# Performance work log

Hardware: AMD Instinct MI355X
Metric: run time of the kernel (lower is better)

The kernel has to match this reference:

```python
import jax, jax.numpy as jnp
import numpy as np


def setup_inputs() -> dict:
    key = jax.random.key(0)
    k1, k2, *kw = jax.random.split(key, 12)
    N, E = 10000, 320000
    D_IN, D_HID, D_EMB, D_PRED = 2, 128, 256, 128

    def lin(k, fan_in, fan_out):
        bound = 1.0 / np.sqrt(fan_in)
        kw_, kb_ = jax.random.split(k)
        W = jax.random.uniform(kw_, (fan_in, fan_out), jnp.float32, -bound, bound)
        b = jax.random.uniform(kb_, (fan_out,), jnp.float32, -bound, bound)
        return W, b

    W1, b1 = lin(kw[0], D_IN, D_HID)
    W2, b2 = lin(kw[1], D_HID, D_EMB)
    Wp1, bp1 = lin(kw[2], D_EMB, D_PRED)
    Wp2, bp2 = lin(kw[3], D_PRED, 1)

    src = jax.random.randint(k1, (E,), 0, N, dtype=jnp.int32)
    dst = jax.random.randint(k2, (E,), 0, N, dtype=jnp.int32)
    return {
        "W1": W1, "b1": b1, "W2": W2, "b2": b2,
        "Wp1": Wp1, "bp1": bp1, "Wp2": Wp2, "bp2": bp2,
        "src": src, "dst": dst, "num_nodes": N,
    }


def reference(W1, b1, W2, b2, Wp1, bp1, Wp2, bp2, src, dst, num_nodes):
    N = num_nodes
    E = src.shape[0]
    ones = jnp.ones((E,), jnp.float32)
    # node features = [in_degree, out_degree]  -> [N, 2]
    in_deg = jax.ops.segment_sum(ones, dst, num_segments=N)
    out_deg = jax.ops.segment_sum(ones, src, num_segments=N)
    x = jnp.stack([in_deg, out_deg], axis=1)

    def gcn_agg(h):
        # sum of messages from source nodes into destination nodes (SpMM-like)
        return jax.ops.segment_sum(h[src], dst, num_segments=N)

    h = jax.nn.relu(gcn_agg(x) @ W1 + b1)        # [N, 128]
    h = gcn_agg(h) @ W2 + b2                     # [N, 256]
    h = jax.nn.relu(h)
    graph_embedding = jnp.sum(h, axis=0)         # [256] (dgl.sum_nodes, single graph)
    m = jax.nn.relu(graph_embedding @ Wp1 + bp1)
    metric = m @ Wp2 + bp2                       # [1]
    return (graph_embedding, metric)
```

## Files before the change

### kernel.cpp

```cpp
#include <hip/hip_runtime.h>

#define N_NODES 10000
#define CAPLOG 7
#define CAP 128
#define NPART 16
#define NBH 128
#define TBH 512
#define TSTRIDE 132
#define HB 128

__global__ __launch_bounds__(TBH) void hist_kernel(const int* __restrict__ src,
                                                   const int* __restrict__ dst,
                                                   uchar2* __restrict__ cnt,
                                                   float* __restrict__ ge_p,
                                                   float* __restrict__ m,
                                                   unsigned int* __restrict__ done,
                                                   int E) {
  __shared__ unsigned int hist[N_NODES];
  const int tid = threadIdx.x, bid = blockIdx.x;
  for (int i = tid; i < N_NODES; i += TBH) hist[i] = 0;
  if (bid < NPART && tid < 256) ge_p[(bid << 8) + tid] = 0.f;
  if (bid == NPART && tid < HB) m[tid] = 0.f;
  if (bid == NPART && tid == HB) *done = 0u;
  __syncthreads();
  const int chunk = (E + NBH - 1) / NBH;
  const int e0 = bid * chunk, e1 = min(E, e0 + chunk);
  for (int e = e0 + tid; e < e1; e += TBH) {
    atomicAdd(&hist[dst[e]], 1u);
    atomicAdd(&hist[src[e]], 0x10000u);
  }
  __syncthreads();
  uchar2* outb = cnt + (size_t)bid * N_NODES;
  for (int i = tid; i < N_NODES; i += TBH) {
    const unsigned v = hist[i];
    outb[i] = make_uchar2((unsigned char)(v & 0xFFFFu), (unsigned char)(v >> 16));
  }
}

__global__ __launch_bounds__(256) void scan_kernel(const uchar2* __restrict__ cnt,
                                                   unsigned char* __restrict__ off,
                                                   unsigned int* __restrict__ pack) {
  const int n = blockIdx.x * 256 + threadIdx.x;
  if (n >= N_NODES) return;
  unsigned run_in = 0, run_out = 0;
#pragma unroll 16
  for (int b = 0; b < NBH; ++b) {
    const uchar2 c = cnt[(size_t)b * N_NODES + n];
    off[(size_t)b * N_NODES + n] = (unsigned char)run_in;
    run_in += c.x;
    run_out += c.y;
  }
  pack[n] = run_in | (run_out << 16);
}

__global__ __launch_bounds__(TBH) void scatter_kernel(const int* __restrict__ src,
                                                      const int* __restrict__ dst,
                                                      const unsigned char* __restrict__ off,
                                                      unsigned short* __restrict__ slots,
                                                      int E) {
  __shared__ unsigned int cur[N_NODES];
  const int tid = threadIdx.x, bid = blockIdx.x;
  const unsigned char* ob = off + (size_t)bid * N_NODES;
  for (int i = tid; i < N_NODES; i += TBH) cur[i] = ob[i];
  __syncthreads();
  const int chunk = (E + NBH - 1) / NBH;
  const int e0 = bid * chunk, e1 = min(E, e0 + chunk);
  for (int e = e0 + tid; e < e1; e += TBH) {
    int d = dst[e];
    unsigned idx = atomicAdd(&cur[d], 1u);
    if (idx < CAP) slots[(d << CAPLOG) + idx] = (unsigned short)src[e];
  }
}

__global__ __launch_bounds__(256) void agg1_kernel(const unsigned int* __restrict__ pack,
                                                   const unsigned short* __restrict__ slots,
                                                   unsigned int* __restrict__ a) {
  const int tid = threadIdx.x;
  const int hw = tid >> 5, hl = tid & 31;
  const int node = blockIdx.x * 8 + hw;
  const int deg = min((int)(pack[node] & 0xFFFFu), CAP);
  const int base = node << CAPLOG;
  unsigned acc = 0u;
  for (int e = hl; e < deg; e += 32) acc += pack[slots[base + e]];
#pragma unroll
  for (int off = 16; off > 0; off >>= 1) acc += (unsigned)__shfl_xor((int)acc, off, 32);
  if (hl == 0) a[node] = acc;
}

#define FMA_ROW(aR0, aR1, aR2, aR3, t)                                       \
  aR0 = fmaf(t.x, w0.x, aR0); aR0 = fmaf(t.y, w1.x, aR0);                    \
  aR0 = fmaf(t.z, w2v.x, aR0); aR0 = fmaf(t.w, w3.x, aR0);                   \
  aR1 = fmaf(t.x, w0.y, aR1); aR1 = fmaf(t.y, w1.y, aR1);                    \
  aR1 = fmaf(t.z, w2v.y, aR1); aR1 = fmaf(t.w, w3.y, aR1);                   \
  aR2 = fmaf(t.x, w0.z, aR2); aR2 = fmaf(t.y, w1.z, aR2);                    \
  aR2 = fmaf(t.z, w2v.z, aR2); aR2 = fmaf(t.w, w3.z, aR2);                   \
  aR3 = fmaf(t.x, w0.w, aR3); aR3 = fmaf(t.y, w1.w, aR3);                    \
  aR3 = fmaf(t.z, w2v.w, aR3); aR3 = fmaf(t.w, w3.w, aR3);

__global__ __launch_bounds__(256, 4) void agg2gemm2_kernel(const unsigned int* __restrict__ pack,
                                                           const unsigned short* __restrict__ slots,
                                                           const unsigned int* __restrict__ a,
                                                           const float* __restrict__ W1,
                                                           const float* __restrict__ b1,
                                                           const float* __restrict__ W2,
                                                           const float* __restrict__ b2,
                                                           float* __restrict__ ge_p) {
  __shared__ float2 s_a[16][CAP + 1];
  __shared__ float s_t[16 * TSTRIDE];
  __shared__ float s_red[4][256];
  const int tid = threadIdx.x, bid = blockIdx.x;
  const int hw = tid >> 5, hl = tid & 31;

#pragma unroll
  for (int nn = 0; nn < 2; ++nn) {
    const int row = hw * 2 + nn;
    const int node = bid * 16 + row;
    const int deg = min((int)(pack[node] & 0xFFFFu), CAP);
    const int base = node << CAPLOG;
    for (int e = hl; e < deg; e += 32) {
      const unsigned v = a[slots[base + e]];
      s_a[row][e] = make_float2((float)(v & 0xFFFFu), (float)(v >> 16));
    }
  }

  float w10[4], w11[4], bb[4];
#pragma unroll
  for (int c = 0; c < 4; ++c) {
    w10[c] = W1[4 * hl + c];
    w11[c] = W1[128 + 4 * hl + c];
    bb[c] = b1[4 * hl + c];
  }
  __syncthreads();

#pragma unroll
  for (int nn = 0; nn < 2; ++nn) {
    const int row = hw * 2 + nn;
    const int node = bid * 16 + row;
    const int deg = min((int)(pack[node] & 0xFFFFu), CAP);
    float acc0 = 0.f, acc1 = 0.f, acc2 = 0.f, acc3 = 0.f;
#pragma unroll 4
    for (int j = 0; j < deg; ++j) {
      const float2 av = s_a[row][j];
      acc0 += fmaxf(fmaf(av.x, w10[0], fmaf(av.y, w11[0], bb[0])), 0.f);
      acc1 += fmaxf(fmaf(av.x, w10[1], fmaf(av.y, w11[1], bb[1])), 0.f);
      acc2 += fmaxf(fmaf(av.x, w10[2], fmaf(av.y, w11[2], bb[2])), 0.f);
      acc3 += fmaxf(fmaf(av.x, w10[3], fmaf(av.y, w11[3], bb[3])), 0.f);
    }
    float* tr = s_t + row * TSTRIDE + 4 * hl;
    tr[0] = acc0; tr[1] = acc1; tr[2] = acc2; tr[3] = acc3;
  }
  __syncthreads();

  const int jq = tid & 63, ng = tid >> 6;
  const int j = jq << 2;
  const float* tb = s_t + (ng << 2) * TSTRIDE;
  float4 wc0 = *(const float4*)(W2 + 0 * 256 + j);
  float4 wc1 = *(const float4*)(W2 + 1 * 256 + j);
  float4 wc2 = *(const float4*)(W2 + 2 * 256 + j);
  float4 wc3 = *(const float4*)(W2 + 3 * 256 + j);
  float a00 = 0.f, a01 = 0.f, a02 = 0.f, a03 = 0.f;
  float a10 = 0.f, a11 = 0.f, a12 = 0.f, a13 = 0.f;
  float a20 = 0.f, a21 = 0.f, a22 = 0.f, a23 = 0.f;
  float a30 = 0.f, a31 = 0.f, a32 = 0.f, a33 = 0.f;
#pragma unroll 4
  for (int k = 0; k < 124; k += 4) {
    const float4 wn0 = *(const float4*)(W2 + (k + 4) * 256 + j);
    const float4 wn1 = *(const float4*)(W2 + (k + 5) * 256 + j);
    const float4 wn2 = *(const float4*)(W2 + (k + 6) * 256 + j);
    const float4 wn3 = *(const float4*)(W2 + (k + 7) * 256 + j);
    const float4 t0 = *(const float4*)(tb + 0 * TSTRIDE + k);
    const float4 t1 = *(const float4*)(tb + 1 * TSTRIDE + k);
    const float4 t2 = *(const float4*)(tb + 2 * TSTRIDE + k);
    const float4 t3 = *(const float4*)(tb + 3 * TSTRIDE + k);
    {
      const float4 w0 = wc0, w1 = wc1, w2v = wc2, w3 = wc3;
      FMA_ROW(a00, a01, a02, a03, t0)
      FMA_ROW(a10, a11, a12, a13, t1)
      FMA_ROW(a20, a21, a22, a23, t2)
      FMA_ROW(a30, a31, a32, a33, t3)
    }
    wc0 = wn0; wc1 = wn1; wc2 = wn2; wc3 = wn3;
  }
  {
    const float4 t0 = *(const float4*)(tb + 0 * TSTRIDE + 124);
    const float4 t1 = *(const float4*)(tb + 1 * TSTRIDE + 124);
    const float4 t2 = *(const float4*)(tb + 2 * TSTRIDE + 124);
    const float4 t3 = *(const float4*)(tb + 3 * TSTRIDE + 124);
    const float4 w0 = wc0, w1 = wc1, w2v = wc2, w3 = wc3;
    FMA_ROW(a00, a01, a02, a03, t0)
    FMA_ROW(a10, a11, a12, a13, t1)
    FMA_ROW(a20, a21, a22, a23, t2)
    FMA_ROW(a30, a31, a32, a33, t3)
  }

  const float4 bj = *(const float4*)(b2 + j);
  float4 part;
  part.x = fmaxf(a00 + bj.x, 0.f) + fmaxf(a10 + bj.x, 0.f) +
           fmaxf(a20 + bj.x, 0.f) + fmaxf(a30 + bj.x, 0.f);
  part.y = fmaxf(a01 + bj.y, 0.f) + fmaxf(a11 + bj.y, 0.f) +
           fmaxf(a21 + bj.y, 0.f) + fmaxf(a31 + bj.y, 0.f);
  part.z = fmaxf(a02 + bj.z, 0.f) + fmaxf(a12 + bj.z, 0.f) +
           fmaxf(a22 + bj.z, 0.f) + fmaxf(a32 + bj.z, 0.f);
  part.w = fmaxf(a03 + bj.w, 0.f) + fmaxf(a13 + bj.w, 0.f) +
           fmaxf(a23 + bj.w, 0.f) + fmaxf(a33 + bj.w, 0.f);
  *(float4*)(&s_red[ng][j]) = part;
  __syncthreads();
  const float g = (s_red[0][tid] + s_red[1][tid]) + (s_red[2][tid] + s_red[3][tid]);
  atomicAdd(&ge_p[((bid & (NPART - 1)) << 8) + tid], g);
}

__global__ __launch_bounds__(256) void head_kernel(const float* __restrict__ ge_p,
                                                   const float* __restrict__ Wp1,
                                                   const float* __restrict__ bp1,
                                                   const float* __restrict__ Wp2,
                                                   const float* __restrict__ bp2,
                                                   float* __restrict__ m,
                                                   unsigned int* __restrict__ done,
                                                   float* __restrict__ out) {
  __shared__ float s_r[4];
  __shared__ int s_last;
  const int tid = threadIdx.x, j = blockIdx.x;
  float g = 0.f;
#pragma unroll
  for (int p = 0; p < NPART; ++p) g += ge_p[p * 256 + tid];
  if (j == 0) out[tid] = g;
  float part = g * Wp1[tid * 128 + j];
#pragma unroll
  for (int o = 32; o > 0; o >>= 1) part += __shfl_xor(part, o);
  if ((tid & 63) == 0) s_r[tid >> 6] = part;
  __syncthreads();
  if (tid == 0) {
    const float mj = bp1[j] + (s_r[0] + s_r[1]) + (s_r[2] + s_r[3]);
    atomicAdd(&m[j], mj);
    __threadfence();
    s_last = (atomicAdd(done, 1u) == HB - 1) ? 1 : 0;
  }
  __syncthreads();
  if (!s_last) return;
  float v = 0.f;
  if (tid < 128)
    v = fmaxf(__hip_atomic_load(&m[tid], __ATOMIC_RELAXED, __HIP_MEMORY_SCOPE_AGENT), 0.f) *
        Wp2[tid];
#pragma unroll
  for (int o = 32; o > 0; o >>= 1) v += __shfl_xor(v, o);
  if ((tid & 63) == 0) s_r[tid >> 6] = v;
  __syncthreads();
  if (tid == 0) out[256] = s_r[0] + s_r[1] + bp2[0];
}

extern "C" void kernel_launch(void* const* d_in, const int* in_sizes, int n_in,
                              void* d_out, int out_size, void* d_ws, size_t ws_size,
                              hipStream_t stream) {
  const float* W1 = (const float*)d_in[0];
  const float* b1 = (const float*)d_in[1];
  const float* W2 = (const float*)d_in[2];
  const float* b2 = (const float*)d_in[3];
  const float* Wp1 = (const float*)d_in[4];
  const float* bp1 = (const float*)d_in[5];
  const float* Wp2 = (const float*)d_in[6];
  const float* bp2 = (const float*)d_in[7];
  const int* src = (const int*)d_in[8];
  const int* dst = (const int*)d_in[9];
  const int E = in_sizes[8];
  const int N = N_NODES;

  char* p = (char*)d_ws;
  float* ge_p = (float*)p;               p += (size_t)NPART * 256 * 4;
  float* m = (float*)p;                  p += HB * 4;
  unsigned int* done = (unsigned int*)p; p += 16;
  unsigned int* pack = (unsigned int*)p; p += (size_t)N * 4;
  unsigned int* a = (unsigned int*)p;    p += (size_t)N * 4;
  unsigned short* slots = (unsigned short*)p; p += (size_t)N * CAP * 2;
  uchar2* cnt = (uchar2*)p;              p += (size_t)NBH * N * 2;
  unsigned char* off = (unsigned char*)p;
  float* out = (float*)d_out;

  hist_kernel<<<NBH, TBH, 0, stream>>>(src, dst, cnt, ge_p, m, done, E);
  scan_kernel<<<(N + 255) / 256, 256, 0, stream>>>(cnt, off, pack);
  scatter_kernel<<<NBH, TBH, 0, stream>>>(src, dst, off, slots, E);
  agg1_kernel<<<N / 8, 256, 0, stream>>>(pack, slots, a);
  agg2gemm2_kernel<<<N / 16, 256, 0, stream>>>(pack, slots, a, W1, b1, W2, b2, ge_p);
  head_kernel<<<HB, 256, 0, stream>>>(ge_p, Wp1, bp1, Wp2, bp2, m, done, out);
}
```

Before: 125.4 us.

## Fuse hist, scan, scatter and agg1 into one persistent kernel with grid barriers

After: 159.1 us. 1.27x slower.

```diff
diff --git a/kernel.cpp b/kernel.cpp
--- a/kernel.cpp
+++ b/kernel.cpp
@@ -9,82 +9,86 @@
 #define TSTRIDE 132
 #define HB 128
 
-__global__ __launch_bounds__(TBH) void hist_kernel(const int* __restrict__ src,
-                                                   const int* __restrict__ dst,
-                                                   uchar2* __restrict__ cnt,
-                                                   float* __restrict__ ge_p,
-                                                   float* __restrict__ m,
-                                                   unsigned int* __restrict__ done,
-                                                   int E) {
-  __shared__ unsigned int hist[N_NODES];
+__device__ __forceinline__ void gridsync(unsigned int* sync, int s, int tid) {
+  __syncthreads();
+  if (tid == 0) {
+    __threadfence();
+    atomicAdd(&sync[s], 1u);
+    while (__hip_atomic_load(&sync[s], __ATOMIC_ACQUIRE, __HIP_MEMORY_SCOPE_AGENT) < NBH) {}
+  }
+  __syncthreads();
+}
+
+__global__ __launch_bounds__(TBH) void build_kernel(const int* __restrict__ src,
+                                                    const int* __restrict__ dst,
+                                                    uchar2* __restrict__ cnt,
+                                                    unsigned char* __restrict__ off,
+                                                    unsigned int* __restrict__ pack,
+                                                    unsigned short* __restrict__ slots,
+                                                    unsigned int* __restrict__ a,
+                                                    unsigned int* __restrict__ sync,
+                                                    int E) {
+  __shared__ unsigned int sh[N_NODES];
   const int tid = threadIdx.x, bid = blockIdx.x;
-  for (int i = tid; i < N_NODES; i += TBH) hist[i] = 0;
-  if (bid < NPART && tid < 256) ge_p[(bid << 8) + tid] = 0.f;
-  if (bid == NPART && tid < HB) m[tid] = 0.f;
-  if (bid == NPART && tid == HB) *done = 0u;
-  __syncthreads();
   const int chunk = (E + NBH - 1) / NBH;
   const int e0 = bid * chunk, e1 = min(E, e0 + chunk);
+
+  for (int i = tid; i < N_NODES; i += TBH) sh[i] = 0;
+  __syncthreads();
   for (int e = e0 + tid; e < e1; e += TBH) {
-    atomicAdd(&hist[dst[e]], 1u);
-    atomicAdd(&hist[src[e]], 0x10000u);
-  }
-  __syncthreads();
-  uchar2* outb = cnt + (size_t)bid * N_NODES;
-  for (int i = tid; i < N_NODES; i += TBH) {
-    const unsigned v = hist[i];
-    outb[i] = make_uchar2((unsigned char)(v & 0xFFFFu), (unsigned char)(v >> 16));
-  }
-}
-
-__global__ __launch_bounds__(256) void scan_kernel(const uchar2* __restrict__ cnt,
-                                                   unsigned char* __restrict__ off,
-                                                   unsigned int* __restrict__ pack) {
-  const int n = blockIdx.x * 256 + threadIdx.x;
-  if (n >= N_NODES) return;
-  unsigned run_in = 0, run_out = 0;
+    atomicAdd(&sh[dst[e]], 1u);
+    atomicAdd(&sh[src[e]], 0x10000u);
+  }
+  __syncthreads();
+  {
+    uchar2* outb = cnt + (size_t)bid * N_NODES;
+    for (int i = tid; i < N_NODES; i += TBH) {
+      const unsigned v = sh[i];
+      outb[i] = make_uchar2((unsigned char)(v & 0xFFFFu), (unsigned char)(v >> 16));
+    }
+  }
+  gridsync(sync, 0, tid);
+
+  {
+    const int n = bid * TBH + tid;
+    if (n < N_NODES) {
+      unsigned run_in = 0, run_out = 0;
 #pragma unroll 16
-  for (int b = 0; b < NBH; ++b) {
-    const uchar2 c = cnt[(size_t)b * N_NODES + n];
-    off[(size_t)b * N_NODES + n] = (unsigned char)run_in;
-    run_in += c.x;
-    run_out += c.y;
-  }
-  pack[n] = run_in | (run_out << 16);
-}
-
-__global__ __launch_bounds__(TBH) void scatter_kernel(const int* __restrict__ src,
-                                                      const int* __restrict__ dst,
-                                                      const unsigned char* __restrict__ off,
-                                                      unsigned short* __restrict__ slots,
-                                                      int E) {
-  __shared__ unsigned int cur[N_NODES];
-  const int tid = threadIdx.x, bid = blockIdx.x;
-  const unsigned char* ob = off + (size_t)bid * N_NODES;
-  for (int i = tid; i < N_NODES; i += TBH) cur[i] = ob[i];
-  __syncthreads();
-  const int chunk = (E + NBH - 1) / NBH;
-  const int e0 = bid * chunk, e1 = min(E, e0 + chunk);
-  for (int e = e0 + tid; e < e1; e += TBH) {
-    int d = dst[e];
-    unsigned idx = atomicAdd(&cur[d], 1u);
-    if (idx < CAP) slots[(d << CAPLOG) + idx] = (unsigned short)src[e];
-  }
-}
-
-__global__ __launch_bounds__(256) void agg1_kernel(const unsigned int* __restrict__ pack,
-                                                   const unsigned short* __restrict__ slots,
-                                                   unsigned int* __restrict__ a) {
-  const int tid = threadIdx.x;
-  const int hw = tid >> 5, hl = tid & 31;
-  const int node = blockIdx.x * 8 + hw;
-  const int deg = min((int)(pack[node] & 0xFFFFu), CAP);
-  const int base = node << CAPLOG;
-  unsigned acc = 0u;
-  for (int e = hl; e < deg; e += 32) acc += pack[slots[base + e]];
-#pragma unroll
-  for (int off = 16; off > 0; off >>= 1) acc += (unsigned)__shfl_xor((int)acc, off, 32);
-  if (hl == 0) a[node] = acc;
+      for (int b = 0; b < NBH; ++b) {
+        const uchar2 c = cnt[(size_t)b * N_NODES + n];
+        off[(size_t)b * N_NODES + n] = (unsigned char)run_in;
+        run_in += c.x;
+        run_out += c.y;
+      }
+      pack[n] = run_in | (run_out << 16);
+    }
+  }
+  gridsync(sync, 1, tid);
+
+  {
+    const unsigned char* ob = off + (size_t)bid * N_NODES;
+    for (int i = tid; i < N_NODES; i += TBH) sh[i] = ob[i];
+    __syncthreads();
+    for (int e = e0 + tid; e < e1; e += TBH) {
+      const int d = dst[e];
+      const unsigned idx = atomicAdd(&sh[d], 1u);
+      if (idx < CAP) slots[(d << CAPLOG) + idx] = (unsigned short)src[e];
+    }
+  }
+  gridsync(sync, 2, tid);
+
+  {
+    const int hwg = bid * 16 + (tid >> 5), hl = tid & 31;
+    for (int node = hwg; node < N_NODES; node += NBH * 16) {
+      const int deg = min((int)(pack[node] & 0xFFFFu), CAP);
+      const int base = node << CAPLOG;
+      unsigned acc = 0u;
+      for (int e = hl; e < deg; e += 32) acc += pack[slots[base + e]];
+#pragma unroll
+      for (int o = 16; o > 0; o >>= 1) acc += (unsigned)__shfl_xor((int)acc, o, 32);
+      if (hl == 0) a[node] = acc;
+    }
+  }
 }
 
 #define FMA_ROW(aR0, aR1, aR2, aR3, t)                                       \
@@ -267,7 +271,9 @@
   char* p = (char*)d_ws;
   float* ge_p = (float*)p;               p += (size_t)NPART * 256 * 4;
   float* m = (float*)p;                  p += HB * 4;
-  unsigned int* done = (unsigned int*)p; p += 16;
+  unsigned int* done = (unsigned int*)p; p += 64;
+  unsigned int* sync = (unsigned int*)p; p += 64;
+  const size_t ctrl_bytes = (size_t)NPART * 256 * 4 + HB * 4 + 128;
   unsigned int* pack = (unsigned int*)p; p += (size_t)N * 4;
   unsigned int* a = (unsigned int*)p;    p += (size_t)N * 4;
   unsigned short* slots = (unsigned short*)p; p += (size_t)N * CAP * 2;
@@ -275,10 +281,8 @@
   unsigned char* off = (unsigned char*)p;
   float* out = (float*)d_out;
 
-  hist_kernel<<<NBH, TBH, 0, stream>>>(src, dst, cnt, ge_p, m, done, E);
-  scan_kernel<<<(N + 255) / 256, 256, 0, stream>>>(cnt, off, pack);
-  scatter_kernel<<<NBH, TBH, 0, stream>>>(src, dst, off, slots, E);
-  agg1_kernel<<<N / 8, 256, 0, stream>>>(pack, slots, a);
+  hipMemsetAsync(d_ws, 0, ctrl_bytes, stream);
+  build_kernel<<<NBH, TBH, 0, stream>>>(src, dst, cnt, off, pack, slots, a, sync, E);
   agg2gemm2_kernel<<<N / 16, 256, 0, stream>>>(pack, slots, a, W1, b1, W2, b2, ge_p);
   head_kernel<<<HB, 256, 0, stream>>>(ge_p, Wp1, bp1, Wp2, bp2, m, done, out);
 }
```
